# Optimization experiments

Hardware: AMD Instinct MI355X
Metric: run time of the kernel (lower is better)

Reference implementation:

```python
import jax, jax.numpy as jnp
import numpy as np
from jax import lax

B, T, D = 4, 2048, 2048
H, K, V = 16, 128, 128
CONV_K = 4
EPS_G = 1e-6
LN_EPS = 1e-5


def _dconv_causal(x, w, b):
    # x: (B,T,C); w: (C,1,Kk) depthwise. torch pads both sides Kk-1 then slices [:T],
    # which equals a causal left-pad of Kk-1.
    y = lax.conv_general_dilated(
        jnp.transpose(x, (0, 2, 1)), w, (1,),
        [(w.shape[-1] - 1, 0)],
        dimension_numbers=('NCH', 'OIH', 'NCH'),
        feature_group_count=w.shape[0])
    return jnp.transpose(y + b[None, :, None], (0, 2, 1))


def _kda_scan(q, k, v, g, beta, scale):
    # q,k: (B,H,T,K); v: (B,H,T,V); g: (B,H,T,K) log-decay (channel-wise); beta: (B,H,T)
    # Gated delta rule: S_t = Diag(exp(g_t)) S_{t-1} + beta_t k_t (v_t - k_t^T Diag(exp(g_t)) S_{t-1})
    S0 = jnp.zeros(q.shape[:2] + (q.shape[-1], v.shape[-1]), q.dtype)

    def step(S, inp):
        qt, kt, vt, gt, bt = inp
        S = S * jnp.exp(gt)[..., :, None]                     # per-key-channel decay
        err = vt - jnp.einsum('bhk,bhkv->bhv', kt, S)         # delta correction
        S = S + bt[..., None, None] * kt[..., None] * err[..., None, :]
        o = scale * jnp.einsum('bhk,bhkv->bhv', qt, S)
        return S, o

    xs = tuple(jnp.moveaxis(t_, 2, 0) for t_ in (q, k, v, g)) + (jnp.moveaxis(beta, 2, 0),)
    _, o = lax.scan(step, S0, xs)
    return jnp.moveaxis(o, 0, 2)                              # (B,H,T,V)


def setup_inputs() -> dict:
    key = jax.random.key(0)
    ks = jax.random.split(key, 16)
    s = 0.02
    return {
        'x':   jax.random.normal(ks[0], (B, T, D), jnp.float32),
        'Wq':  jax.random.normal(ks[1], (H * K, D), jnp.float32) * s,
        'Wk':  jax.random.normal(ks[2], (H * K, D), jnp.float32) * s,
        'Wv':  jax.random.normal(ks[3], (H * V, D), jnp.float32) * s,
        'Wa':  jax.random.normal(ks[4], (H * V, D), jnp.float32) * s,
        'ba':  jax.random.normal(ks[5], (H * V,), jnp.float32) * s,
        'Wb':  jax.random.normal(ks[6], (H, D), jnp.float32) * s,
        'bb':  jax.random.normal(ks[7], (H,), jnp.float32) * s,
        'Wg':  jax.random.normal(ks[8], (H * V, D), jnp.float32) * s,
        'Wo':  jax.random.normal(ks[9], (D, H * V), jnp.float32) * s,
        'cqw': jax.random.normal(ks[10], (H * K, 1, CONV_K), jnp.float32) * 0.2,
        'cqb': jnp.zeros((H * K,), jnp.float32),
        'ckw': jax.random.normal(ks[11], (H * K, 1, CONV_K), jnp.float32) * 0.2,
        'ckb': jnp.zeros((H * K,), jnp.float32),
        'cvw': jax.random.normal(ks[12], (H * V, 1, CONV_K), jnp.float32) * 0.2,
        'cvb': jnp.zeros((H * V,), jnp.float32),
        'ln_w': jnp.ones((V,), jnp.float32),
        'ln_b': jnp.zeros((V,), jnp.float32),
    }


def reference(x, Wq, Wk, Wv, Wa, ba, Wb, bb, Wg, Wo,
              cqw, cqb, ckw, ckb, cvw, cvb, ln_w, ln_b):
    b, t, _ = x.shape
    scale = K ** -0.5
    q = jax.nn.silu(_dconv_causal(x @ Wq.T, cqw, cqb))
    k = jax.nn.silu(_dconv_causal(x @ Wk.T, ckw, ckb))
    v = jax.nn.silu(_dconv_causal(x @ Wv.T, cvw, cvb))
    q = q.reshape(b, t, H, K).transpose(0, 2, 1, 3)           # (B,H,T,K)
    k = k.reshape(b, t, H, K).transpose(0, 2, 1, 3)
    v = v.reshape(b, t, H, V).transpose(0, 2, 1, 3)
    a = jax.nn.sigmoid(x @ Wa.T + ba).reshape(b, t, H, V).transpose(0, 2, 1, 3)
    g = jnp.log(jnp.maximum(a, EPS_G))                        # log-space channel gate
    beta = jax.nn.sigmoid(x @ Wb.T + bb).transpose(0, 2, 1)   # (B,H,T)
    o = _kda_scan(q, k, v, g, beta, scale).transpose(0, 2, 1, 3)  # (B,T,H,V)
    mu = o.mean(-1, keepdims=True)
    var = ((o - mu) ** 2).mean(-1, keepdims=True)
    o = (o - mu) * lax.rsqrt(var + LN_EPS) * ln_w + ln_b      # per-head LayerNorm
    gate = jax.nn.sigmoid(x @ Wg.T).reshape(b, t, H, V)
    return ((o * gate).reshape(b, t, H * V)) @ Wo.T
```

## Files before the change

kernel.cpp:

```cpp
#include <hip/hip_runtime.h>
#include <cstdint>
#include <cstddef>

#define B_ 4
#define T_ 2048
#define D_ 2048
#define H_ 16

typedef __bf16 bf16x8 __attribute__((ext_vector_type(8)));
typedef float  f32x4  __attribute__((ext_vector_type(4)));
typedef unsigned short u16;
typedef u16 u16x8 __attribute__((ext_vector_type(8)));

__device__ __forceinline__ u16 f2bf(float f) {
    union { float f; unsigned u; } v; v.f = f;
    unsigned r = v.u + 0x7FFFu + ((v.u >> 16) & 1u);
    return (u16)(r >> 16);
}
__device__ __forceinline__ float bf2f(u16 h) {
    union { unsigned u; float f; } v; v.u = ((unsigned)h) << 16;
    return v.f;
}
__device__ __forceinline__ float sigmoidf_(float x) {
    return 1.f / (1.f + __expf(-x));
}
__device__ __forceinline__ void async_load16(const void* g, void* l) {
    __builtin_amdgcn_global_load_lds(
        (const __attribute__((address_space(1))) void*)g,
        (__attribute__((address_space(3))) void*)l,
        16, 0, 0);
}

__device__ __forceinline__ float row_allreduce16(float x) {
    int v;
    v = __builtin_amdgcn_update_dpp(0, __builtin_bit_cast(int, x), 0xB1, 0xF, 0xF, true);
    x += __builtin_bit_cast(float, v);
    v = __builtin_amdgcn_update_dpp(0, __builtin_bit_cast(int, x), 0x4E, 0xF, 0xF, true);
    x += __builtin_bit_cast(float, v);
    v = __builtin_amdgcn_update_dpp(0, __builtin_bit_cast(int, x), 0x140, 0xF, 0xF, true);
    x += __builtin_bit_cast(float, v);
    v = __builtin_amdgcn_update_dpp(0, __builtin_bit_cast(int, x), 0x141, 0xF, 0xF, true);
    x += __builtin_bit_cast(float, v);
    return x;
}

__device__ __forceinline__ float grp32_allreduce(float x) {
    x = row_allreduce16(x);
    x += __shfl_xor(x, 32);
    return x;
}

__global__ void cvt_bf16_k(const float* __restrict__ s, u16* __restrict__ d, int n) {
    int i = blockIdx.x * 256 + threadIdx.x;
    if (i < n) d[i] = f2bf(s[i]);
}

__global__ void pad_wb_k(const float* __restrict__ Wb, u16* __restrict__ d) {
    int i = blockIdx.x * 256 + threadIdx.x;
    d[i] = (i < 32768) ? f2bf(Wb[i]) : (u16)0;
}

__device__ __forceinline__ void store_c(float* p, float v) { *p = v; }
__device__ __forceinline__ void store_c(u16* p, float v) { *p = f2bf(v); }

template <typename OutT, int PERM>
__global__ __launch_bounds__(256) void gemm_bt(const u16* __restrict__ A,
                                               const u16* __restrict__ Bm,
                                               OutT* __restrict__ C, int K, int ldc) {
    __shared__ __align__(16) u16 smA[128 * 64];
    __shared__ __align__(16) u16 smB[128 * 64];
    const int tid  = threadIdx.x;
    const int lane = tid & 63;
    const int w    = tid >> 6;
    const int wm   = (w >> 1) * 64;
    const int wn   = (w & 1) * 64;
    const int bm   = blockIdx.x, bn = blockIdx.y;

    f32x4 acc[4][4];
#pragma unroll
    for (int i = 0; i < 4; ++i)
#pragma unroll
        for (int j = 0; j < 4; ++j) acc[i][j] = (f32x4){0.f, 0.f, 0.f, 0.f};

    const int rr = tid >> 3;
    const int cc = (tid & 7) * 8;
    const u16* Ag = A + (size_t)(bm * 128) * K;
    const u16* Bg = Bm + (size_t)(bn * 128) * K;

    for (int k0 = 0; k0 < K; k0 += 64) {
#pragma unroll
        for (int it = 0; it < 4; ++it) {
            async_load16(Ag + (size_t)(it * 32 + rr) * K + (k0 + cc), &smA[(it * 256 + tid) * 8]);
            async_load16(Bg + (size_t)(it * 32 + rr) * K + (k0 + cc), &smB[(it * 256 + tid) * 8]);
        }
        __syncthreads();
#pragma unroll
        for (int kk = 0; kk < 64; kk += 32) {
            bf16x8 af[4], bfr[4];
            const int qoff = kk + ((lane >> 4) * 8);
#pragma unroll
            for (int mi = 0; mi < 4; ++mi)
                af[mi] = *(const bf16x8*)&smA[(wm + mi * 16 + (lane & 15)) * 64 + qoff];
#pragma unroll
            for (int ni = 0; ni < 4; ++ni)
                bfr[ni] = *(const bf16x8*)&smB[(wn + ni * 16 + (lane & 15)) * 64 + qoff];
#pragma unroll
            for (int mi = 0; mi < 4; ++mi)
#pragma unroll
                for (int ni = 0; ni < 4; ++ni)
                    acc[mi][ni] = __builtin_amdgcn_mfma_f32_16x16x32_bf16(af[mi], bfr[ni], acc[mi][ni], 0, 0, 0);
        }
        __syncthreads();
    }

#pragma unroll
    for (int mi = 0; mi < 4; ++mi) {
        const int row0 = bm * 128 + wm + mi * 16 + ((lane >> 4) * 4);
#pragma unroll
        for (int ni = 0; ni < 4; ++ni) {
            int colg = bn * 128 + wn + ni * 16 + (lane & 15);
            if (PERM) {
                int cl = colg & 127;
                colg = (colg & ~127) | (((cl & 31) << 2) | (cl >> 5));
            }
#pragma unroll
            for (int rg = 0; rg < 4; ++rg)
                store_c(&C[(size_t)(row0 + rg) * ldc + colg], acc[mi][ni][rg]);
        }
    }
}

template <int TRANSPOSE>
__global__ void conv_silu_k(const u16* __restrict__ pre,
                            const float* __restrict__ w, const float* __restrict__ bias,
                            u16* __restrict__ outp) {
    int idx = blockIdx.x * 256 + threadIdx.x;
    int c = idx & 2047;
    int t = (idx >> 11) & (T_ - 1);
    int b = idx >> 22;
    const u16* base = pre + (size_t)(b * T_ + t) * 2048 + c;
    float acc = bias[c];
#pragma unroll
    for (int j = 0; j < 4; ++j) {
        int tt = t - 3 + j;
        if (tt >= 0) {
            float xv = bf2f(base[(ptrdiff_t)(j - 3) * 2048]);
            acc = fmaf(xv, w[c * 4 + j], acc);
        }
    }
    float y = acc * sigmoidf_(acc);
    int h = c >> 7, cl = c & 127;
    int p = TRANSPOSE ? (((cl & 31) << 2) | (cl >> 5)) : cl;
    outp[((size_t)(b * H_ + h) * T_ + t) * 128 + p] = f2bf(y);
}

#define TB2 16
__global__ __launch_bounds__(512, 4) void kda_scan_k(const u16* __restrict__ qg,
                                                     const u16* __restrict__ kg,
                                                     const u16* __restrict__ vg,
                                                     const u16* __restrict__ ag,
                                                     const u16* __restrict__ bpg,
                                                     const float* __restrict__ bav,
                                                     const float* __restrict__ bbv,
                                                     u16* __restrict__ og) {
    const int blk = blockIdx.x;
    const int bh  = (blk & 7) * 8 + (blk >> 6);
    const int vch = (blk >> 3) & 7;
    const int tid = threadIdx.x;
    const int lane = tid & 63;
    const int w    = tid >> 6;
    const int colIdx = w * 2 + ((lane >> 4) & 1);
    const int kidx   = (lane & 15) + ((lane >> 5) << 4);
    const int b = bh >> 4, h = bh & 15;

    __shared__ __align__(16) float sq[2][TB2][128];
    __shared__ __align__(16) float sk[2][TB2][128];
    __shared__ __align__(16) float sd[2][TB2][128];
    __shared__ float sv[2][TB2][16];
    __shared__ float sb_[2][TB2];

    const u16* qb  = qg + (size_t)bh * T_ * 128;
    const u16* kb  = kg + (size_t)bh * T_ * 128;
    const u16* vb  = vg + (size_t)bh * T_ * 128 + vch * 16;
    const u16* ab  = ag + (size_t)b * T_ * 2048 + h * 128;
    const u16* bpb = bpg + (size_t)b * T_ * 128 + h;
    u16* op = og + (size_t)b * T_ * 2048 + h * 128 + vch * 16 + colIdx;

    const int ur = tid >> 5;
    const int p4 = (tid & 31) * 4;
    const float rba0 = bav[h * 128 +  0 + (tid & 31)];
    const float rba1 = bav[h * 128 + 32 + (tid & 31)];
    const float rba2 = bav[h * 128 + 64 + (tid & 31)];
    const float rba3 = bav[h * 128 + 96 + (tid & 31)];
    const float bbh = bbv[h];

    float S[4];
#pragma unroll
    for (int j = 0; j < 4; ++j) S[j] = 0.f;

    ushort4 rq, rk, ra;
    float rv = 0.f, rbet = 0.f;
    rq = *(const ushort4*)(qb + (size_t)ur * 128 + p4);
    rk = *(const ushort4*)(kb + (size_t)ur * 128 + p4);
    ra = *(const ushort4*)(ab + (size_t)ur * 2048 + p4);
    if (tid < 256) rv = bf2f(vb[(size_t)(tid >> 4) * 128 + (tid & 15)]);
    if (tid < TB2) rbet = bf2f(bpb[(size_t)tid * 128]);

    const float scale = 0.08838834764831845f;
    const int NM = T_ / TB2;
    for (int m = 0; m < NM; ++m) {
        const int pb = m & 1;
        float4 fq = {bf2f(rq.x), bf2f(rq.y), bf2f(rq.z), bf2f(rq.w)};
        float4 fk = {bf2f(rk.x), bf2f(rk.y), bf2f(rk.z), bf2f(rk.w)};
        float4 fd = {fmaxf(sigmoidf_(bf2f(ra.x) + rba0), 1e-6f),
                     fmaxf(sigmoidf_(bf2f(ra.y) + rba1), 1e-6f),
                     fmaxf(sigmoidf_(bf2f(ra.z) + rba2), 1e-6f),
                     fmaxf(sigmoidf_(bf2f(ra.w) + rba3), 1e-6f)};
        *(float4*)&sq[pb][ur][p4] = fq;
        *(float4*)&sk[pb][ur][p4] = fk;
        *(float4*)&sd[pb][ur][p4] = fd;
        if (tid < 256) sv[pb][tid >> 4][tid & 15] = rv;
        if (tid < TB2) sb_[pb][tid] = sigmoidf_(rbet + bbh);
        __syncthreads();
        if (m + 1 < NM) {
            size_t t0n = (size_t)(m + 1) * TB2;
            rq = *(const ushort4*)(qb + (t0n + ur) * 128 + p4);
            rk = *(const ushort4*)(kb + (t0n + ur) * 128 + p4);
            ra = *(const ushort4*)(ab + (t0n + ur) * 2048 + p4);
            if (tid < 256) rv = bf2f(vb[(t0n + (tid >> 4)) * 128 + (tid & 15)]);
            if (tid < TB2) rbet = bf2f(bpb[(t0n + tid) * 128]);
        }
#pragma unroll
        for (int u = 0; u < TB2; ++u) {
            float4 q4 = *(const float4*)&sq[pb][u][kidx * 4];
            float4 k4 = *(const float4*)&sk[pb][u][kidx * 4];
            float4 d4 = *(const float4*)&sd[pb][u][kidx * 4];
            float e0, e1;
            S[0] *= d4.x; e0 = k4.x * S[0];
            S[1] *= d4.y; e1 = k4.y * S[1];
            S[2] *= d4.z; e0 = fmaf(k4.z, S[2], e0);
            S[3] *= d4.w; e1 = fmaf(k4.w, S[3], e1);
            float errp = grp32_allreduce(e0 + e1);
            float uu = sb_[pb][u] * (sv[pb][u][colIdx] - errp);
            float o0, o1;
            S[0] = fmaf(k4.x, uu, S[0]); o0 = q4.x * S[0];
            S[1] = fmaf(k4.y, uu, S[1]); o1 = q4.y * S[1];
            S[2] = fmaf(k4.z, uu, S[2]); o0 = fmaf(q4.z, S[2], o0);
            S[3] = fmaf(k4.w, uu, S[3]); o1 = fmaf(q4.w, S[3], o1);
            float outv = grp32_allreduce(o0 + o1);
            if (((lane & 15) | (lane >> 5)) == 0)
                op[(size_t)(m * TB2 + u) * 2048] = f2bf(scale * outv);
        }
        __syncthreads();
    }
}

__global__ __launch_bounds__(256) void ln_gate_k(const u16* __restrict__ o,
                                                 const u16* __restrict__ gpre,
                                                 const float* __restrict__ lnw,
                                                 const float* __restrict__ lnb,
                                                 u16* __restrict__ act) {
    int inst = blockIdx.x * 4 + (threadIdx.x >> 6);
    int lane = threadIdx.x & 63;
    int bt = inst >> 4, h = inst & 15;
    const u16* opr = o + (size_t)bt * 2048 + h * 128;
    ushort2 xr = *(const ushort2*)(opr + lane * 2);
    float x0 = bf2f(xr.x), x1 = bf2f(xr.y);
    float s  = x0 + x1;
    float ss = x0 * x0 + x1 * x1;
#pragma unroll
    for (int msk = 1; msk < 64; msk <<= 1) {
        s  += __shfl_xor(s, msk);
        ss += __shfl_xor(ss, msk);
    }
    float mu   = s * (1.f / 128.f);
    float var  = ss * (1.f / 128.f) - mu * mu;
    float rstd = rsqrtf(var + 1e-5f);
    const u16* gp = gpre + (size_t)bt * 2048 + h * 128 + lane * 2;
    u16* ap = act + (size_t)bt * 2048 + h * 128 + lane * 2;
#pragma unroll
    for (int e = 0; e < 2; ++e) {
        int v = lane * 2 + e;
        float xx = (e == 0) ? x0 : x1;
        float y = (xx - mu) * rstd * lnw[v] + lnb[v];
        float gate = sigmoidf_(bf2f(gp[e]));
        ap[e] = f2bf(y * gate);
    }
}

extern "C" void kernel_launch(void* const* d_in, const int* in_sizes, int n_in,
                              void* d_out, int out_size, void* d_ws, size_t ws_size,
                              hipStream_t stream) {
    (void)in_sizes; (void)n_in; (void)out_size; (void)ws_size;
    const float* x   = (const float*)d_in[0];
    const float* Wq  = (const float*)d_in[1];
    const float* Wk  = (const float*)d_in[2];
    const float* Wv  = (const float*)d_in[3];
    const float* Wa  = (const float*)d_in[4];
    const float* ba  = (const float*)d_in[5];
    const float* Wb  = (const float*)d_in[6];
    const float* bbv = (const float*)d_in[7];
    const float* Wg  = (const float*)d_in[8];
    const float* Wo  = (const float*)d_in[9];
    const float* cqw = (const float*)d_in[10];
    const float* cqb = (const float*)d_in[11];
    const float* ckw = (const float*)d_in[12];
    const float* ckb = (const float*)d_in[13];
    const float* cvw = (const float*)d_in[14];
    const float* cvb = (const float*)d_in[15];
    const float* lnw = (const float*)d_in[16];
    const float* lnb = (const float*)d_in[17];
    float* out = (float*)d_out;

    char* p = (char*)d_ws;
    size_t off = 0;
    auto take = [&](size_t bytes) -> char* {
        char* r = p + off;
        off += (bytes + 255) & ~(size_t)255;
        return r;
    };
    u16* Wslot = (u16*)take((size_t)4194304 * 2);
    u16* qpre  = (u16*)take((size_t)16777216 * 2);
    u16* kpre  = (u16*)take((size_t)16777216 * 2);
    u16* vpre  = (u16*)take((size_t)16777216 * 2);
    u16* apre  = (u16*)take((size_t)16777216 * 2);
    u16* bpre  = (u16*)take((size_t)1048576 * 2);

    u16* xb  = (u16*)d_out;
    u16* qsc = (u16*)d_out + 16777216;
    u16* ksc  = qpre;
    u16* vsc  = kpre;
    u16* ob   = vpre;
    u16* gpre = qpre;
    u16* act  = kpre;

    cvt_bf16_k<<<65536, 256, 0, stream>>>(x, xb, 16777216);

    cvt_bf16_k<<<16384, 256, 0, stream>>>(Wq, Wslot, 4194304);
    gemm_bt<u16, 0><<<dim3(64, 16), 256, 0, stream>>>(xb, Wslot, qpre, 2048, 2048);
    cvt_bf16_k<<<16384, 256, 0, stream>>>(Wk, Wslot, 4194304);
    gemm_bt<u16, 0><<<dim3(64, 16), 256, 0, stream>>>(xb, Wslot, kpre, 2048, 2048);
    cvt_bf16_k<<<16384, 256, 0, stream>>>(Wv, Wslot, 4194304);
    gemm_bt<u16, 0><<<dim3(64, 16), 256, 0, stream>>>(xb, Wslot, vpre, 2048, 2048);
    cvt_bf16_k<<<16384, 256, 0, stream>>>(Wa, Wslot, 4194304);
    gemm_bt<u16, 1><<<dim3(64, 16), 256, 0, stream>>>(xb, Wslot, apre, 2048, 2048);
    pad_wb_k<<<1024, 256, 0, stream>>>(Wb, Wslot);
    gemm_bt<u16, 0><<<dim3(64, 1), 256, 0, stream>>>(xb, Wslot, bpre, 2048, 128);

    conv_silu_k<1><<<65536, 256, 0, stream>>>(qpre, cqw, cqb, qsc);
    conv_silu_k<1><<<65536, 256, 0, stream>>>(kpre, ckw, ckb, ksc);
    conv_silu_k<0><<<65536, 256, 0, stream>>>(vpre, cvw, cvb, vsc);

    kda_scan_k<<<512, 512, 0, stream>>>(qsc, ksc, vsc, apre, bpre, ba, bbv, ob);

    cvt_bf16_k<<<16384, 256, 0, stream>>>(Wg, Wslot, 4194304);
    gemm_bt<u16, 0><<<dim3(64, 16), 256, 0, stream>>>(xb, Wslot, gpre, 2048, 2048);

    ln_gate_k<<<32768, 256, 0, stream>>>(ob, gpre, lnw, lnb, act);

    cvt_bf16_k<<<16384, 256, 0, stream>>>(Wo, Wslot, 4194304);
    gemm_bt<float, 0><<<dim3(64, 16), 256, 0, stream>>>(act, Wslot, out, 2048, 2048);
}
```

Before: 1.800 ms.

## Stream q/k/v per-thread from global in scan, vectorize bf16 conversion

The scan kernel no longer stages q, k and v through shared memory. Each thread keeps a 4-deep rolling register prefetch of its own q/k slice and v column, loaded straight from global memory four timesteps ahead. Only the decay gate and beta still go through LDS. This cuts shared-memory traffic and LDS footprint in the latency-bound recurrent loop, but adds many small per-step global loads that depend on cache hits. Separately, the fp32-to-bf16 conversion kernel now handles four elements per thread with vector loads and stores, and its grids are shrunk to match.

```diff
diff --git a/kernel.cpp b/kernel.cpp
--- a/kernel.cpp
+++ b/kernel.cpp
@@ -52,7 +52,11 @@
 
 __global__ void cvt_bf16_k(const float* __restrict__ s, u16* __restrict__ d, int n) {
     int i = blockIdx.x * 256 + threadIdx.x;
-    if (i < n) d[i] = f2bf(s[i]);
+    if (i * 4 < n) {
+        float4 v = *(const float4*)(s + (size_t)i * 4);
+        ushort4 o = {f2bf(v.x), f2bf(v.y), f2bf(v.z), f2bf(v.w)};
+        *(ushort4*)(d + (size_t)i * 4) = o;
+    }
 }
 
 __global__ void pad_wb_k(const float* __restrict__ Wb, u16* __restrict__ d) {
@@ -173,15 +177,12 @@
     const int kidx   = (lane & 15) + ((lane >> 5) << 4);
     const int b = bh >> 4, h = bh & 15;
 
-    __shared__ __align__(16) float sq[2][TB2][128];
-    __shared__ __align__(16) float sk[2][TB2][128];
     __shared__ __align__(16) float sd[2][TB2][128];
-    __shared__ float sv[2][TB2][16];
     __shared__ float sb_[2][TB2];
 
-    const u16* qb  = qg + (size_t)bh * T_ * 128;
-    const u16* kb  = kg + (size_t)bh * T_ * 128;
-    const u16* vb  = vg + (size_t)bh * T_ * 128 + vch * 16;
+    const u16* qb  = qg + (size_t)bh * T_ * 128 + kidx * 4;
+    const u16* kb  = kg + (size_t)bh * T_ * 128 + kidx * 4;
+    const u16* vb  = vg + (size_t)bh * T_ * 128 + vch * 16 + colIdx;
     const u16* ab  = ag + (size_t)b * T_ * 2048 + h * 128;
     const u16* bpb = bpg + (size_t)b * T_ * 128 + h;
     u16* op = og + (size_t)b * T_ * 2048 + h * 128 + vch * 16 + colIdx;
@@ -198,50 +199,54 @@
 #pragma unroll
     for (int j = 0; j < 4; ++j) S[j] = 0.f;
 
-    ushort4 rq, rk, ra;
-    float rv = 0.f, rbet = 0.f;
-    rq = *(const ushort4*)(qb + (size_t)ur * 128 + p4);
-    rk = *(const ushort4*)(kb + (size_t)ur * 128 + p4);
-    ra = *(const ushort4*)(ab + (size_t)ur * 2048 + p4);
-    if (tid < 256) rv = bf2f(vb[(size_t)(tid >> 4) * 128 + (tid & 15)]);
-    if (tid < TB2) rbet = bf2f(bpb[(size_t)tid * 128]);
+    ushort4 rq4[4], rk4[4];
+    u16 rv4[4];
+#pragma unroll
+    for (int i = 0; i < 4; ++i) {
+        rq4[i] = *(const ushort4*)(qb + (size_t)i * 128);
+        rk4[i] = *(const ushort4*)(kb + (size_t)i * 128);
+        rv4[i] = vb[(size_t)i * 128];
+    }
+
+    ushort4 ra = *(const ushort4*)(ab + (size_t)ur * 2048 + p4);
+    float rbet = (tid < TB2) ? bf2f(bpb[(size_t)tid * 128]) : 0.f;
 
     const float scale = 0.08838834764831845f;
     const int NM = T_ / TB2;
     for (int m = 0; m < NM; ++m) {
         const int pb = m & 1;
-        float4 fq = {bf2f(rq.x), bf2f(rq.y), bf2f(rq.z), bf2f(rq.w)};
-        float4 fk = {bf2f(rk.x), bf2f(rk.y), bf2f(rk.z), bf2f(rk.w)};
         float4 fd = {fmaxf(sigmoidf_(bf2f(ra.x) + rba0), 1e-6f),
                      fmaxf(sigmoidf_(bf2f(ra.y) + rba1), 1e-6f),
                      fmaxf(sigmoidf_(bf2f(ra.z) + rba2), 1e-6f),
                      fmaxf(sigmoidf_(bf2f(ra.w) + rba3), 1e-6f)};
-        *(float4*)&sq[pb][ur][p4] = fq;
-        *(float4*)&sk[pb][ur][p4] = fk;
         *(float4*)&sd[pb][ur][p4] = fd;
-        if (tid < 256) sv[pb][tid >> 4][tid & 15] = rv;
         if (tid < TB2) sb_[pb][tid] = sigmoidf_(rbet + bbh);
         __syncthreads();
         if (m + 1 < NM) {
             size_t t0n = (size_t)(m + 1) * TB2;
-            rq = *(const ushort4*)(qb + (t0n + ur) * 128 + p4);
-            rk = *(const ushort4*)(kb + (t0n + ur) * 128 + p4);
             ra = *(const ushort4*)(ab + (t0n + ur) * 2048 + p4);
-            if (tid < 256) rv = bf2f(vb[(t0n + (tid >> 4)) * 128 + (tid & 15)]);
             if (tid < TB2) rbet = bf2f(bpb[(t0n + tid) * 128]);
         }
 #pragma unroll
         for (int u = 0; u < TB2; ++u) {
-            float4 q4 = *(const float4*)&sq[pb][u][kidx * 4];
-            float4 k4 = *(const float4*)&sk[pb][u][kidx * 4];
+            const int s = u & 3;
+            const int t = m * TB2 + u;
+            float4 q4 = {bf2f(rq4[s].x), bf2f(rq4[s].y), bf2f(rq4[s].z), bf2f(rq4[s].w)};
+            float4 k4 = {bf2f(rk4[s].x), bf2f(rk4[s].y), bf2f(rk4[s].z), bf2f(rk4[s].w)};
+            float fv = bf2f(rv4[s]);
             float4 d4 = *(const float4*)&sd[pb][u][kidx * 4];
+            int tn = t + 4; if (tn > T_ - 1) tn = T_ - 1;
+            rq4[s] = *(const ushort4*)(qb + (size_t)tn * 128);
+            rk4[s] = *(const ushort4*)(kb + (size_t)tn * 128);
+            rv4[s] = vb[(size_t)tn * 128];
+
             float e0, e1;
             S[0] *= d4.x; e0 = k4.x * S[0];
             S[1] *= d4.y; e1 = k4.y * S[1];
             S[2] *= d4.z; e0 = fmaf(k4.z, S[2], e0);
             S[3] *= d4.w; e1 = fmaf(k4.w, S[3], e1);
             float errp = grp32_allreduce(e0 + e1);
-            float uu = sb_[pb][u] * (sv[pb][u][colIdx] - errp);
+            float uu = sb_[pb][u] * (fv - errp);
             float o0, o1;
             S[0] = fmaf(k4.x, uu, S[0]); o0 = q4.x * S[0];
             S[1] = fmaf(k4.y, uu, S[1]); o1 = q4.y * S[1];
@@ -249,7 +254,7 @@
             S[3] = fmaf(k4.w, uu, S[3]); o1 = fmaf(q4.w, S[3], o1);
             float outv = grp32_allreduce(o0 + o1);
             if (((lane & 15) | (lane >> 5)) == 0)
-                op[(size_t)(m * TB2 + u) * 2048] = f2bf(scale * outv);
+                op[(size_t)t * 2048] = f2bf(scale * outv);
         }
         __syncthreads();
     }
@@ -334,15 +339,15 @@
     u16* gpre = qpre;
     u16* act  = kpre;
 
-    cvt_bf16_k<<<65536, 256, 0, stream>>>(x, xb, 16777216);
-
-    cvt_bf16_k<<<16384, 256, 0, stream>>>(Wq, Wslot, 4194304);
+    cvt_bf16_k<<<16384, 256, 0, stream>>>(x, xb, 16777216);
+
+    cvt_bf16_k<<<4096, 256, 0, stream>>>(Wq, Wslot, 4194304);
     gemm_bt<u16, 0><<<dim3(64, 16), 256, 0, stream>>>(xb, Wslot, qpre, 2048, 2048);
-    cvt_bf16_k<<<16384, 256, 0, stream>>>(Wk, Wslot, 4194304);
+    cvt_bf16_k<<<4096, 256, 0, stream>>>(Wk, Wslot, 4194304);
     gemm_bt<u16, 0><<<dim3(64, 16), 256, 0, stream>>>(xb, Wslot, kpre, 2048, 2048);
-    cvt_bf16_k<<<16384, 256, 0, stream>>>(Wv, Wslot, 4194304);
+    cvt_bf16_k<<<4096, 256, 0, stream>>>(Wv, Wslot, 4194304);
     gemm_bt<u16, 0><<<dim3(64, 16), 256, 0, stream>>>(xb, Wslot, vpre, 2048, 2048);
-    cvt_bf16_k<<<16384, 256, 0, stream>>>(Wa, Wslot, 4194304);
+    cvt_bf16_k<<<4096, 256, 0, stream>>>(Wa, Wslot, 4194304);
     gemm_bt<u16, 1><<<dim3(64, 16), 256, 0, stream>>>(xb, Wslot, apre, 2048, 2048);
     pad_wb_k<<<1024, 256, 0, stream>>>(Wb, Wslot);
     gemm_bt<u16, 0><<<dim3(64, 1), 256, 0, stream>>>(xb, Wslot, bpre, 2048, 128);
@@ -353,11 +358,11 @@
 
     kda_scan_k<<<512, 512, 0, stream>>>(qsc, ksc, vsc, apre, bpre, ba, bbv, ob);
 
-    cvt_bf16_k<<<16384, 256, 0, stream>>>(Wg, Wslot, 4194304);
+    cvt_bf16_k<<<4096, 256, 0, stream>>>(Wg, Wslot, 4194304);
     gemm_bt<u16, 0><<<dim3(64, 16), 256, 0, stream>>>(xb, Wslot, gpre, 2048, 2048);
 
     ln_gate_k<<<32768, 256, 0, stream>>>(ob, gpre, lnw, lnb, act);
 
-    cvt_bf16_k<<<16384, 256, 0, stream>>>(Wo, Wslot, 4194304);
+    cvt_bf16_k<<<4096, 256, 0, stream>>>(Wo, Wslot, 4194304);
     gemm_bt<float, 0><<<dim3(64, 16), 256, 0, stream>>>(act, Wslot, out, 2048, 2048);
 }
```

Result: slower. 1.880 ms (+4.4%).
